# Optimization experiments

Measured on AMD Instinct MI355X. Metric: run time of the kernel, lower is better.

## Reference

```python
import jax, jax.numpy as jnp
import numpy as np

S, B, H, NH = 2048, 2, 1024, 16
HD = H // NH  # 64


def setup_inputs() -> dict:
    key = jax.random.key(0)
    ks = jax.random.split(key, 8)
    w = 0.02
    return {
        "hidden_states": jax.random.normal(ks[0], (S, B, H), jnp.float32),
        "attn_mask": jax.random.normal(ks[1], (1, NH, S, S), jnp.float32),
        "attention_mask": jax.random.normal(ks[2], (B * NH, 1, S), jnp.float32),
        "Wq": jax.random.normal(ks[3], (H, H), jnp.float32) * w,
        "bq": jnp.zeros((H,), jnp.float32),
        "Wk": jax.random.normal(ks[4], (H, H), jnp.float32) * w,
        "bk": jnp.zeros((H,), jnp.float32),
        "Wv": jax.random.normal(ks[5], (H, H), jnp.float32) * w,
        "bv": jnp.zeros((H,), jnp.float32),
        "Wo": jax.random.normal(ks[6], (H, H), jnp.float32) * w,
        "bo": jnp.zeros((H,), jnp.float32),
    }


def _split_heads(x):
    # [S, B, H] -> [B*NH, S, HD]  (matches torch reshape(S, B*NH, HD).transpose(0,1))
    return jnp.transpose(x.reshape(S, B * NH, HD), (1, 0, 2))


def reference(hidden_states, attn_mask, attention_mask, Wq, bq, Wk, bk, Wv, bv, Wo, bo):
    scale = 1.0 / jnp.sqrt(jnp.asarray(HD, hidden_states.dtype))
    q = _split_heads((hidden_states @ Wq.T + bq) * scale)  # [B*NH, S, HD]
    k = _split_heads(hidden_states @ Wk.T + bk)
    v = _split_heads(hidden_states @ Wv.T + bv)

    scores = jnp.einsum("nsd,ntd->nst", q, k)  # [B*NH, S, S]
    scores = (scores.reshape(B, NH, S, S) + attn_mask).reshape(B * NH, S, S)
    scores = scores + attention_mask  # broadcast over query dim

    probs = jax.nn.softmax(scores, axis=-1)  # dropout p=0 (eval)
    ctx = jnp.einsum("nst,ntd->nsd", probs, v)  # [B*NH, S, HD]
    ctx = jnp.transpose(ctx, (1, 0, 2)).reshape(S, B, H)
    return ctx @ Wo.T + bo
```

## Files before the change

### kernel.cpp

```cpp
#include <hip/hip_runtime.h>
#include <hip/hip_bf16.h>
#include <math.h>

#define S_LEN 2048
#define BATCH 2
#define HID 1024
#define NHEAD 16
#define HDIM 64
#define NTOK (S_LEN*BATCH)

typedef __bf16 bf16;
typedef __bf16 bf16x4 __attribute__((ext_vector_type(4)));
typedef __bf16 bf16x8 __attribute__((ext_vector_type(8)));
typedef float f32x4 __attribute__((ext_vector_type(4)));

typedef const __attribute__((address_space(1))) unsigned int* gptr_t;
typedef __attribute__((address_space(3))) unsigned int* lptr_t;

__device__ __forceinline__ void gload16(const void* g, void* l) {
    __builtin_amdgcn_global_load_lds((gptr_t)g, (lptr_t)l, 16, 0, 0);
}

__global__ void cvt_f32_bf16(const float* __restrict__ src, bf16* __restrict__ dst, int n) {
    int i = (blockIdx.x * blockDim.x + threadIdx.x) * 8;
    if (i >= n) return;
    const float4* s = (const float4*)(src + i);
    float4 a = s[0], b = s[1];
    bf16x8 o;
    o[0] = (bf16)a.x; o[1] = (bf16)a.y; o[2] = (bf16)a.z; o[3] = (bf16)a.w;
    o[4] = (bf16)b.x; o[5] = (bf16)b.y; o[6] = (bf16)b.z; o[7] = (bf16)b.w;
    *(bf16x8*)(dst + i) = o;
}

#define BM 128
#define BN 128
#define BK 32

__global__ __launch_bounds__(256) void gemm_bt(
    const bf16* __restrict__ A, const bf16* __restrict__ B,
    int M, int N, int K, int mode,
    const float* __restrict__ bq, const float* __restrict__ bk,
    const float* __restrict__ bv, const float* __restrict__ bo,
    bf16* __restrict__ qh, bf16* __restrict__ kh, bf16* __restrict__ vT,
    float* __restrict__ outp)
{
    __shared__ __align__(16) bf16 As[BM * BK];
    __shared__ __align__(16) bf16 Bs[BN * BK];
    const int tid = threadIdx.x;
    const int lane = tid & 63, wv = tid >> 6;
    const int g = lane >> 4, l15 = lane & 15;
    const int wr = wv >> 1, wc = wv & 1;
    const int bm = blockIdx.y * BM, bn = blockIdx.x * BN;

    f32x4 zero4 = {0.f, 0.f, 0.f, 0.f};
    f32x4 acc[4][4];
#pragma unroll
    for (int mi = 0; mi < 4; mi++)
#pragma unroll
        for (int ni = 0; ni < 4; ni++) acc[mi][ni] = zero4;

    const int r0 = wv * 32 + (lane >> 2);
    const int c0 = (lane & 3) * 8;
    const bf16* Ag0 = A + (size_t)(bm + r0) * K + c0;
    const bf16* Ag1 = Ag0 + (size_t)16 * K;
    const bf16* Bg0 = B + (size_t)(bn + r0) * K + c0;
    const bf16* Bg1 = Bg0 + (size_t)16 * K;
    bf16* AsW = &As[(wv * 32) * BK];
    bf16* BsW = &Bs[(wv * 32) * BK];

    for (int k0 = 0; k0 < K; k0 += BK) {
        gload16(Ag0 + k0, AsW);
        gload16(Ag1 + k0, AsW + 16 * BK);
        gload16(Bg0 + k0, BsW);
        gload16(Bg1 + k0, BsW + 16 * BK);
        __syncthreads();

        bf16x8 aF[4], bF[4];
#pragma unroll
        for (int mi = 0; mi < 4; mi++)
            aF[mi] = *(const bf16x8*)&As[(wr * 64 + mi * 16 + l15) * BK + g * 8];
#pragma unroll
        for (int ni = 0; ni < 4; ni++)
            bF[ni] = *(const bf16x8*)&Bs[(wc * 64 + ni * 16 + l15) * BK + g * 8];
#pragma unroll
        for (int mi = 0; mi < 4; mi++)
#pragma unroll
            for (int ni = 0; ni < 4; ni++)
                acc[mi][ni] = __builtin_amdgcn_mfma_f32_16x16x32_bf16(
                    aF[mi], bF[ni], acc[mi][ni], 0, 0, 0);
        __syncthreads();
    }

    if (mode == 0) {
#pragma unroll
        for (int ni = 0; ni < 4; ni++) {
            int n = bn + wc * 64 + ni * 16 + l15;
            int which = n >> 10;
            int c = n & 1023;
            int nh = c >> 6, d = c & 63;
            const float* bias_p = (which == 0) ? bq : (which == 1) ? bk : bv;
            float bias = bias_p[c];
            float scl = (which == 0) ? 0.125f : 1.0f;
#pragma unroll
            for (int mi = 0; mi < 4; mi++) {
#pragma unroll
                for (int r = 0; r < 4; r++) {
                    int m = bm + wr * 64 + mi * 16 + g * 4 + r;
                    int s = m >> 1, b = m & 1;
                    int head = b * NHEAD + nh;
                    bf16 val = (bf16)((acc[mi][ni][r] + bias) * scl);
                    if (which == 2)
                        vT[((size_t)(head * HDIM + d)) * S_LEN + s] = val;
                    else {
                        bf16* dst = (which == 0) ? qh : kh;
                        dst[((size_t)(head * S_LEN + s)) * HDIM + d] = val;
                    }
                }
            }
        }
    } else {
#pragma unroll
        for (int ni = 0; ni < 4; ni++) {
            int n = bn + wc * 64 + ni * 16 + l15;
            float bias = bo[n];
#pragma unroll
            for (int mi = 0; mi < 4; mi++) {
#pragma unroll
                for (int r = 0; r < 4; r++) {
                    int m = bm + wr * 64 + mi * 16 + g * 4 + r;
                    outp[(size_t)m * HID + n] = acc[mi][ni][r] + bias;
                }
            }
        }
    }
}

__global__ __launch_bounds__(256) void attn(
    const bf16* __restrict__ q, const bf16* __restrict__ kh, const bf16* __restrict__ vT,
    const float* __restrict__ amask,
    const float* __restrict__ kmask,
    bf16* __restrict__ ctx)
{
    __shared__ __align__(16) bf16 KS[2][64 * 64];
    __shared__ __align__(16) bf16 VS[2][64 * 64];
    __shared__ __align__(16) float MS[32 * 64];
    __shared__ __align__(16) float KM[256];
    __shared__ __align__(16) bf16 P[4][16 * 72];

    const int tid = threadIdx.x, lane = tid & 63, wv = tid >> 6;
    const int g = lane >> 4, l15 = lane & 15;
    const int b = wv >> 1, stsub = wv & 1;

    const int hw = blockIdx.y * 64 + blockIdx.x;
    const int vid = (hw & 7) * 128 + (hw >> 3);
    const int nh = vid >> 6;
    const int qt = vid & 63;
    const int st0 = qt * 32;
    const int st0s = st0 + stsub * 16;
    const int n = b * NHEAD + nh;

    const bf16* qrow = q + ((size_t)(n * S_LEN + st0s + l15)) * HDIM;
    bf16x8 bQ0 = *(const bf16x8*)(qrow + g * 8);
    bf16x8 bQ1 = *(const bf16x8*)(qrow + 32 + g * 8);

    const int krow = lane >> 3;
    const int kc8 = (lane & 7) ^ (krow & 7);
    const int bsel = wv & 1;
    const bf16* kvsrc;
    size_t kvstride;
    if (wv < 2) {
        kvsrc = kh + ((size_t)(bsel * NHEAD + nh) * S_LEN + krow) * HDIM + kc8 * 8;
        kvstride = (size_t)8 * HDIM;
    } else {
        kvsrc = vT + ((size_t)(bsel * NHEAD + nh) * HDIM + krow) * S_LEN + kc8 * 8;
        kvstride = (size_t)8 * S_LEN;
    }
    bf16* kvdst = (wv < 2) ? &KS[bsel][0] : &VS[bsel][0];
    const int mrowA = 8 * wv + (lane >> 4);
    const int mrowB = mrowA + 4;
    const int mcA = (lane & 15) ^ ((mrowA & 7) << 1);
    const int mcB = (lane & 15) ^ ((mrowB & 7) << 1);
    const float* msrcA = amask + ((size_t)nh * S_LEN + st0 + mrowA) * S_LEN + mcA * 4;
    const float* msrcB = amask + ((size_t)nh * S_LEN + st0 + mrowB) * S_LEN + mcB * 4;
    float* mdstA = MS + (8 * wv) * 64;
    float* mdstB = MS + (8 * wv + 4) * 64;
    const int kmb_ = (lane >> 4) & 1;
    const float* kmsrc = kmask + (size_t)(kmb_ * NHEAD + nh) * S_LEN + (lane & 15) * 4;

    f32x4 zero4 = {0.f, 0.f, 0.f, 0.f};
    f32x4 O[4];
#pragma unroll
    for (int t = 0; t < 4; t++) O[t] = zero4;
    float mrun = -1e30f, lrun = 0.f;

    const int pk8 = l15 & 7;
    const int mr = stsub * 16 + l15;

#pragma unroll 1
    for (int it = 0; it < 32; ++it) {
        const int tt = it * 64;
#pragma unroll
        for (int j = 0; j < 8; ++j)
            gload16(kvsrc + tt * (wv < 2 ? HDIM : 1) + j * kvstride, kvdst + j * 512);
        gload16(msrcA + tt, mdstA);
        gload16(msrcB + tt, mdstB);
        if (wv == 0) gload16(kmsrc + tt, KM);
        __syncthreads();

        f32x4 sc[4];
#pragma unroll
        for (int c = 0; c < 4; c++) {
            bf16x8 aK0 = *(const bf16x8*)&KS[b][(16 * c + l15) * 64 + (g ^ pk8) * 8];
            bf16x8 aK1 = *(const bf16x8*)&KS[b][(16 * c + l15) * 64 + ((g + 4) ^ pk8) * 8];
            f32x4 s = zero4;
            s = __builtin_amdgcn_mfma_f32_16x16x32_bf16(aK0, bQ0, s, 0, 0, 0);
            s = __builtin_amdgcn_mfma_f32_16x16x32_bf16(aK1, bQ1, s, 0, 0, 0);
            sc[c] = s;
        }
#pragma unroll
        for (int c = 0; c < 4; c++) {
            int physm = (4 * c + g) ^ ((mr & 7) << 1);
            f32x4 mk = *(const f32x4*)&MS[mr * 64 + physm * 4];
            f32x4 km = *(const f32x4*)&KM[b * 64 + (4 * c + g) * 4];
            sc[c] += mk + km;
        }
        float cm = fmaxf(fmaxf(fmaxf(sc[0][0], sc[0][1]), fmaxf(sc[0][2], sc[0][3])),
                         fmaxf(fmaxf(sc[1][0], sc[1][1]), fmaxf(sc[1][2], sc[1][3])));
        cm = fmaxf(cm, fmaxf(fmaxf(fmaxf(sc[2][0], sc[2][1]), fmaxf(sc[2][2], sc[2][3])),
                             fmaxf(fmaxf(sc[3][0], sc[3][1]), fmaxf(sc[3][2], sc[3][3]))));
        cm = fmaxf(cm, __shfl_xor(cm, 16, 64));
        cm = fmaxf(cm, __shfl_xor(cm, 32, 64));
        if (!__all(cm - mrun <= 8.0f)) {
            float mn = fmaxf(mrun, cm);
            float f = __expf(mrun - mn);
            mrun = mn;
            lrun *= f;
#pragma unroll
            for (int r = 0; r < 4; r++) {
                float fb = __shfl(f, 4 * g + r, 64);
#pragma unroll
                for (int dt = 0; dt < 4; dt++) O[dt][r] *= fb;
            }
        }
        float rs = 0.f;
#pragma unroll
        for (int c = 0; c < 4; c++)
#pragma unroll
            for (int r = 0; r < 4; r++) {
                float p = __expf(sc[c][r] - mrun);
                sc[c][r] = p;
                rs += p;
            }
        rs += __shfl_xor(rs, 16, 64);
        rs += __shfl_xor(rs, 32, 64);
        lrun += rs;
#pragma unroll
        for (int c = 0; c < 4; c++) {
            bf16x4 pk;
            pk[0] = (bf16)sc[c][0]; pk[1] = (bf16)sc[c][1];
            pk[2] = (bf16)sc[c][2]; pk[3] = (bf16)sc[c][3];
            *(bf16x4*)&P[wv][l15 * 72 + 16 * c + 4 * g] = pk;
        }
        bf16x8 aP0 = *(const bf16x8*)&P[wv][l15 * 72 + g * 8];
        bf16x8 aP1 = *(const bf16x8*)&P[wv][l15 * 72 + 32 + g * 8];
#pragma unroll
        for (int dt = 0; dt < 4; dt++) {
            bf16x8 bV0 = *(const bf16x8*)&VS[b][(dt * 16 + l15) * 64 + (g ^ pk8) * 8];
            bf16x8 bV1 = *(const bf16x8*)&VS[b][(dt * 16 + l15) * 64 + ((g + 4) ^ pk8) * 8];
            O[dt] = __builtin_amdgcn_mfma_f32_16x16x32_bf16(aP0, bV0, O[dt], 0, 0, 0);
            O[dt] = __builtin_amdgcn_mfma_f32_16x16x32_bf16(aP1, bV1, O[dt], 0, 0, 0);
        }
        __syncthreads();
    }

#pragma unroll
    for (int r = 0; r < 4; r++) {
        float lq = __shfl(lrun, 4 * g + r, 64);
        float inv = 1.0f / lq;
        int s = st0s + 4 * g + r;
        int token = s * BATCH + b;
#pragma unroll
        for (int dt = 0; dt < 4; dt++) {
            int h = nh * HDIM + dt * 16 + l15;
            ctx[(size_t)token * HID + h] = (bf16)(O[dt][r] * inv);
        }
    }
}

extern "C" void kernel_launch(void* const* d_in, const int* in_sizes, int n_in,
                              void* d_out, int out_size, void* d_ws, size_t ws_size,
                              hipStream_t stream) {
    const float* hidden = (const float*)d_in[0];
    const float* amask  = (const float*)d_in[1];
    const float* kmask  = (const float*)d_in[2];
    const float* Wq = (const float*)d_in[3];
    const float* bq = (const float*)d_in[4];
    const float* Wk = (const float*)d_in[5];
    const float* bk = (const float*)d_in[6];
    const float* Wv = (const float*)d_in[7];
    const float* bv = (const float*)d_in[8];
    const float* Wo = (const float*)d_in[9];
    const float* bo = (const float*)d_in[10];
    float* out = (float*)d_out;

    char* ws = (char*)d_ws;
    bf16* Xb   = (bf16*)(ws);
    bf16* Wcat = (bf16*)(ws + (8u  << 20));
    bf16* Wob  = (bf16*)(ws + (14u << 20));
    bf16* qh   = (bf16*)(ws + (16u << 20));
    bf16* kh   = (bf16*)(ws + (24u << 20));
    bf16* vT   = (bf16*)(ws + (32u << 20));
    bf16* ctx  = (bf16*)(ws + (40u << 20));

    cvt_f32_bf16<<<2048, 256, 0, stream>>>(hidden, Xb, NTOK * HID);
    cvt_f32_bf16<<<512, 256, 0, stream>>>(Wq, Wcat,              HID * HID);
    cvt_f32_bf16<<<512, 256, 0, stream>>>(Wk, Wcat + HID * HID,  HID * HID);
    cvt_f32_bf16<<<512, 256, 0, stream>>>(Wv, Wcat + 2 * HID * HID, HID * HID);
    cvt_f32_bf16<<<512, 256, 0, stream>>>(Wo, Wob, HID * HID);

    gemm_bt<<<dim3(24, 32), 256, 0, stream>>>(Xb, Wcat, NTOK, 3 * HID, HID, 0,
                                              bq, bk, bv, bo, qh, kh, vT, nullptr);
    attn<<<dim3(64, 16), 256, 0, stream>>>(qh, kh, vT, amask, kmask, ctx);
    gemm_bt<<<dim3(8, 32), 256, 0, stream>>>(ctx, Wob, NTOK, HID, HID, 1,
                                             bq, bk, bv, bo, qh, kh, vT, out);
}
```

Baseline: 255.0 us.

## Double-buffer K/V/mask tiles and remap blocks to single batch per block

Each block now serves 64 query rows of one batch instead of 32 rows of both batches, so every wave handles 16 rows of the same head. The K, V, attention-mask and key-mask tiles are double-buffered in LDS. The next tile is issued with global_load_lds before computing on the current one, using explicit vmcnt waits and raw barriers in place of __syncthreads. This overlaps global loads with MFMA and softmax work. In exchange, LDS use roughly doubles, which may reduce occupancy, and the K/V tiles are no longer shared across the two batches within a block.

```diff
diff --git a/kernel.cpp b/kernel.cpp
--- a/kernel.cpp
+++ b/kernel.cpp
@@ -19,6 +19,9 @@
 
 __device__ __forceinline__ void gload16(const void* g, void* l) {
     __builtin_amdgcn_global_load_lds((gptr_t)g, (lptr_t)l, 16, 0, 0);
+}
+__device__ __forceinline__ void gload4(const void* g, void* l) {
+    __builtin_amdgcn_global_load_lds((gptr_t)g, (lptr_t)l, 4, 0, 0);
 }
 
 __global__ void cvt_f32_bf16(const float* __restrict__ src, bf16* __restrict__ dst, int n) {
@@ -143,49 +146,38 @@
 {
     __shared__ __align__(16) bf16 KS[2][64 * 64];
     __shared__ __align__(16) bf16 VS[2][64 * 64];
-    __shared__ __align__(16) float MS[32 * 64];
-    __shared__ __align__(16) float KM[256];
+    __shared__ __align__(16) float MS[2][64 * 64];
+    __shared__ __align__(16) float KM[2][64];
     __shared__ __align__(16) bf16 P[4][16 * 72];
 
     const int tid = threadIdx.x, lane = tid & 63, wv = tid >> 6;
     const int g = lane >> 4, l15 = lane & 15;
-    const int b = wv >> 1, stsub = wv & 1;
 
     const int hw = blockIdx.y * 64 + blockIdx.x;
     const int vid = (hw & 7) * 128 + (hw >> 3);
     const int nh = vid >> 6;
-    const int qt = vid & 63;
-    const int st0 = qt * 32;
-    const int st0s = st0 + stsub * 16;
+    const int qt = (vid & 63) >> 1;
+    const int b  = vid & 1;
+    const int st0 = qt * 64;
+    const int st0s = st0 + wv * 16;
     const int n = b * NHEAD + nh;
 
     const bf16* qrow = q + ((size_t)(n * S_LEN + st0s + l15)) * HDIM;
     bf16x8 bQ0 = *(const bf16x8*)(qrow + g * 8);
     bf16x8 bQ1 = *(const bf16x8*)(qrow + 32 + g * 8);
 
-    const int krow = lane >> 3;
-    const int kc8 = (lane & 7) ^ (krow & 7);
-    const int bsel = wv & 1;
-    const bf16* kvsrc;
-    size_t kvstride;
-    if (wv < 2) {
-        kvsrc = kh + ((size_t)(bsel * NHEAD + nh) * S_LEN + krow) * HDIM + kc8 * 8;
-        kvstride = (size_t)8 * HDIM;
-    } else {
-        kvsrc = vT + ((size_t)(bsel * NHEAD + nh) * HDIM + krow) * S_LEN + kc8 * 8;
-        kvstride = (size_t)8 * S_LEN;
-    }
-    bf16* kvdst = (wv < 2) ? &KS[bsel][0] : &VS[bsel][0];
-    const int mrowA = 8 * wv + (lane >> 4);
-    const int mrowB = mrowA + 4;
-    const int mcA = (lane & 15) ^ ((mrowA & 7) << 1);
-    const int mcB = (lane & 15) ^ ((mrowB & 7) << 1);
-    const float* msrcA = amask + ((size_t)nh * S_LEN + st0 + mrowA) * S_LEN + mcA * 4;
-    const float* msrcB = amask + ((size_t)nh * S_LEN + st0 + mrowB) * S_LEN + mcB * 4;
-    float* mdstA = MS + (8 * wv) * 64;
-    float* mdstB = MS + (8 * wv + 4) * 64;
-    const int kmb_ = (lane >> 4) & 1;
-    const float* kmsrc = kmask + (size_t)(kmb_ * NHEAD + nh) * S_LEN + (lane & 15) * 4;
+    const int r8 = lane >> 3;
+    const int c8 = (lane & 7) ^ r8;
+    const bf16* ksrc = kh + ((size_t)n * S_LEN + 16 * wv + r8) * HDIM + c8 * 8;
+    const bf16* vsrc = vT + ((size_t)n * HDIM + 16 * wv + r8) * S_LEN + c8 * 8;
+    const float* msrcJ[4];
+#pragma unroll
+    for (int j = 0; j < 4; j++) {
+        int row = 16 * wv + 4 * j + (lane >> 4);
+        int col16 = (lane & 15) ^ ((row & 7) << 1);
+        msrcJ[j] = amask + ((size_t)nh * S_LEN + st0 + row) * S_LEN + col16 * 4;
+    }
+    const float* kmsrc = kmask + (size_t)n * S_LEN + lane;
 
     f32x4 zero4 = {0.f, 0.f, 0.f, 0.f};
     f32x4 O[4];
@@ -194,24 +186,41 @@
     float mrun = -1e30f, lrun = 0.f;
 
     const int pk8 = l15 & 7;
-    const int mr = stsub * 16 + l15;
+    const int mrr = wv * 16 + l15;
+
+#define STAGE(bb, tt)                                                          \
+    do {                                                                       \
+        gload16(ksrc + (size_t)(tt) * HDIM, &KS[bb][(16 * wv) * 64]);          \
+        gload16(ksrc + (size_t)((tt) + 8) * HDIM, &KS[bb][(16 * wv + 8) * 64]);\
+        gload16(vsrc + (tt), &VS[bb][(16 * wv) * 64]);                         \
+        gload16(vsrc + (size_t)8 * S_LEN + (tt), &VS[bb][(16 * wv + 8) * 64]); \
+        gload16(msrcJ[0] + (tt), &MS[bb][(16 * wv) * 64]);                     \
+        gload16(msrcJ[1] + (tt), &MS[bb][(16 * wv + 4) * 64]);                 \
+        gload16(msrcJ[2] + (tt), &MS[bb][(16 * wv + 8) * 64]);                 \
+        gload16(msrcJ[3] + (tt), &MS[bb][(16 * wv + 12) * 64]);                \
+        gload4(kmsrc + (tt), &KM[bb][0]);                                      \
+    } while (0)
+
+    STAGE(0, 0);
 
 #pragma unroll 1
     for (int it = 0; it < 32; ++it) {
-        const int tt = it * 64;
-#pragma unroll
-        for (int j = 0; j < 8; ++j)
-            gload16(kvsrc + tt * (wv < 2 ? HDIM : 1) + j * kvstride, kvdst + j * 512);
-        gload16(msrcA + tt, mdstA);
-        gload16(msrcB + tt, mdstB);
-        if (wv == 0) gload16(kmsrc + tt, KM);
-        __syncthreads();
+        const int cur = it & 1;
+        __builtin_amdgcn_s_barrier();
+        if (it < 31) {
+            STAGE(cur ^ 1, (it + 1) * 64);
+            asm volatile("s_waitcnt vmcnt(9)" ::: "memory");
+        } else {
+            asm volatile("s_waitcnt vmcnt(0)" ::: "memory");
+        }
+        __builtin_amdgcn_s_barrier();
+        __builtin_amdgcn_sched_barrier(0);
 
         f32x4 sc[4];
 #pragma unroll
         for (int c = 0; c < 4; c++) {
-            bf16x8 aK0 = *(const bf16x8*)&KS[b][(16 * c + l15) * 64 + (g ^ pk8) * 8];
-            bf16x8 aK1 = *(const bf16x8*)&KS[b][(16 * c + l15) * 64 + ((g + 4) ^ pk8) * 8];
+            bf16x8 aK0 = *(const bf16x8*)&KS[cur][(16 * c + l15) * 64 + (g ^ pk8) * 8];
+            bf16x8 aK1 = *(const bf16x8*)&KS[cur][(16 * c + l15) * 64 + ((g + 4) ^ pk8) * 8];
             f32x4 s = zero4;
             s = __builtin_amdgcn_mfma_f32_16x16x32_bf16(aK0, bQ0, s, 0, 0, 0);
             s = __builtin_amdgcn_mfma_f32_16x16x32_bf16(aK1, bQ1, s, 0, 0, 0);
@@ -219,9 +228,9 @@
         }
 #pragma unroll
         for (int c = 0; c < 4; c++) {
-            int physm = (4 * c + g) ^ ((mr & 7) << 1);
-            f32x4 mk = *(const f32x4*)&MS[mr * 64 + physm * 4];
-            f32x4 km = *(const f32x4*)&KM[b * 64 + (4 * c + g) * 4];
+            int physm = (4 * c + g) ^ ((mrr & 7) << 1);
+            f32x4 mk = *(const f32x4*)&MS[cur][mrr * 64 + physm * 4];
+            f32x4 km = *(const f32x4*)&KM[cur][(4 * c + g) * 4];
             sc[c] += mk + km;
         }
         float cm = fmaxf(fmaxf(fmaxf(sc[0][0], sc[0][1]), fmaxf(sc[0][2], sc[0][3])),
@@ -265,13 +274,13 @@
         bf16x8 aP1 = *(const bf16x8*)&P[wv][l15 * 72 + 32 + g * 8];
 #pragma unroll
         for (int dt = 0; dt < 4; dt++) {
-            bf16x8 bV0 = *(const bf16x8*)&VS[b][(dt * 16 + l15) * 64 + (g ^ pk8) * 8];
-            bf16x8 bV1 = *(const bf16x8*)&VS[b][(dt * 16 + l15) * 64 + ((g + 4) ^ pk8) * 8];
+            bf16x8 bV0 = *(const bf16x8*)&VS[cur][(dt * 16 + l15) * 64 + (g ^ pk8) * 8];
+            bf16x8 bV1 = *(const bf16x8*)&VS[cur][(dt * 16 + l15) * 64 + ((g + 4) ^ pk8) * 8];
             O[dt] = __builtin_amdgcn_mfma_f32_16x16x32_bf16(aP0, bV0, O[dt], 0, 0, 0);
             O[dt] = __builtin_amdgcn_mfma_f32_16x16x32_bf16(aP1, bV1, O[dt], 0, 0, 0);
         }
-        __syncthreads();
-    }
+    }
+#undef STAGE
 
 #pragma unroll
     for (int r = 0; r < 4; r++) {
```

After: 239.7 us. 6.0% less time.
